# Kernel optimization log

Measured on AMD Instinct MI355X. Metric: run time of the kernel, lower is better.

Reference implementation:

```python
import jax, jax.numpy as jnp
from jax import lax
import numpy as np

SHAPE = (50, 60, 65)   # -> after net: (17, 27, 32), flatten = 14688
NEG = 0.01             # LeakyReLU default slope
B, N = 8, 80000        # batch size, total active voxels


def _lrelu(x):
    return jnp.where(x >= 0, x, NEG * x)


def _sparse_conv(x, w, b, m):
    # Regular (non-submanifold) sparse conv == dense VALID conv on densified
    # input (inactive sites are 0 so they contribute nothing). Output site is
    # active iff any input site in the kernel footprint is active; bias is
    # added only at active output sites.
    k = w.shape[2]
    y = lax.conv_general_dilated(x, w, (1, 1, 1), 'VALID',
                                 dimension_numbers=('NCDHW', 'OIDHW', 'NCDHW'))
    m2 = lax.reduce_window(m, 0.0, lax.max, (1, 1, k, k, k), (1, 1, 1, 1, 1), 'VALID')
    y = jnp.where(m2 > 0, y + b[None, :, None, None, None], 0.0)
    return y, m2


def _sparse_maxpool(x, m, k):
    # spconv SparseMaxPool: max over ACTIVE sites only (inactive excluded, not 0)
    xm = jnp.where(m > 0, x, -jnp.inf)
    p = lax.reduce_window(xm, -jnp.inf, lax.max, (1, 1, k, k, k), (1, 1, 1, 1, 1), 'VALID')
    m2 = lax.reduce_window(m, 0.0, lax.max, (1, 1, k, k, k), (1, 1, 1, 1, 1), 'VALID')
    return jnp.where(m2 > 0, p, 0.0), m2


def setup_inputs() -> dict:
    key = jax.random.key(0)
    ks = jax.random.split(key, 24)
    D, H, W = SHAPE
    features = jax.random.normal(ks[0], (N, 1), dtype=jnp.float32)
    bi = jax.random.randint(ks[1], (N,), 0, B)
    zi = jax.random.randint(ks[2], (N,), 0, D)
    yi = jax.random.randint(ks[3], (N,), 0, H)
    xi = jax.random.randint(ks[4], (N,), 0, W)
    coors = jnp.stack([bi, zi, yi, xi], axis=1).astype(jnp.int32)
    s = 0.05
    p = {}
    p['w1'] = jax.random.normal(ks[5], (32, 1, 4, 4, 4), jnp.float32) * s
    p['b1'] = jax.random.normal(ks[6], (32,), jnp.float32) * s
    p['w2'] = jax.random.normal(ks[7], (32, 32, 4, 4, 4), jnp.float32) * s
    p['b2'] = jax.random.normal(ks[8], (32,), jnp.float32) * s
    p['w3'] = jax.random.normal(ks[9], (32, 32, 4, 4, 4), jnp.float32) * s
    p['b3'] = jax.random.normal(ks[10], (32,), jnp.float32) * s
    p['w4'] = jax.random.normal(ks[11], (32, 32, 4, 4, 4), jnp.float32) * s
    p['b4'] = jax.random.normal(ks[12], (32,), jnp.float32) * s
    p['w5'] = jax.random.normal(ks[13], (32, 32, 4, 4, 4), jnp.float32) * s
    p['b5'] = jax.random.normal(ks[14], (32,), jnp.float32) * s
    p['w6'] = jax.random.normal(ks[15], (32, 32, 4, 4, 4), jnp.float32) * s
    p['b6'] = jax.random.normal(ks[16], (32,), jnp.float32) * s
    p['w7'] = jax.random.normal(ks[17], (1, 32, 4, 4, 4), jnp.float32) * s
    p['b7'] = jax.random.normal(ks[18], (1,), jnp.float32) * s
    p['W8'] = jax.random.normal(ks[19], (14688, 1000), jnp.float32) * 0.01
    p['b8'] = jax.random.normal(ks[20], (1000,), jnp.float32) * s
    p['W9'] = jax.random.normal(ks[21], (1000, 1000), jnp.float32) * 0.03
    p['b9'] = jax.random.normal(ks[22], (1000,), jnp.float32) * s
    p['W10'] = jax.random.normal(ks[23], (1000, 1), jnp.float32) * 0.03
    p['b10'] = jnp.zeros((1,), jnp.float32)
    return dict(features=features, coors=coors, batch_size=B, **p)


def reference(features, coors, batch_size,
              w1, b1, w2, b2, w3, b3, w4, b4, w5, b5, w6, b6, w7, b7,
              W8, b8, W9, b9, W10, b10):
    D, H, W = SHAPE
    bi, zi, yi, xi = coors[:, 0], coors[:, 1], coors[:, 2], coors[:, 3]
    dense = jnp.zeros((batch_size, 1, D, H, W), features.dtype)
    dense = dense.at[bi, 0, zi, yi, xi].set(features[:, 0])
    mask = jnp.zeros((batch_size, 1, D, H, W), features.dtype)
    mask = mask.at[bi, 0, zi, yi, xi].set(1.0)

    x, m = _sparse_conv(dense, w1, b1, mask); x = _lrelu(x)
    x, m = _sparse_conv(x, w2, b2, m);        x = _lrelu(x)
    x, m = _sparse_maxpool(x, m, 5)
    x, m = _sparse_conv(x, w3, b3, m);        x = _lrelu(x)
    x, m = _sparse_conv(x, w4, b4, m);        x = _lrelu(x)
    x, m = _sparse_maxpool(x, m, 5)
    x, m = _sparse_conv(x, w5, b5, m);        x = _lrelu(x)
    x, m = _sparse_conv(x, w6, b6, m);        x = _lrelu(x)
    x, m = _sparse_conv(x, w7, b7, m);        x = _lrelu(x)
    x, m = _sparse_maxpool(x, m, 5)

    # ToDense (inactive sites already 0) + Flatten -> [B, 14688]
    h = x.reshape(x.shape[0], -1)
    h = _lrelu(h @ W8 + b8)
    h = _lrelu(h @ W9 + b9)
    out = _lrelu(h @ W10 + b10)
    return out
```

## Files before the change

### kernel.cpp

```cpp
#include <hip/hip_runtime.h>
#include <cstddef>


#define NEGSLOPE 0.01f
#define NINF (-3.0e38f)

#define TZ 4
#define TY 4
#define TXT 16
#define IZ 7
#define IY 7
#define IX 19
#define NV (IZ*IY*IX)

typedef __attribute__((ext_vector_type(8)))  short  short8;
typedef __attribute__((ext_vector_type(16))) float  floatx16;

__device__ __forceinline__ float lrelu(float v) { return v >= 0.f ? v : NEGSLOPE * v; }

__device__ __forceinline__ unsigned short f2bf(float f) {
  unsigned b = __float_as_uint(f);
  return (unsigned short)((b + 0x7fffu + ((b >> 16) & 1u)) >> 16);
}
__device__ __forceinline__ float bf2f(unsigned short h) {
  return __uint_as_float(((unsigned)h) << 16);
}
__device__ __forceinline__ unsigned splitpair(float a, float b, unsigned& lo) {
  unsigned short ha = f2bf(a), hb = f2bf(b);
  unsigned short la = f2bf(a - bf2f(ha)), lb = f2bf(b - bf2f(hb));
  lo = (unsigned)la | ((unsigned)lb << 16);
  return (unsigned)ha | ((unsigned)hb << 16);
}

__global__ void k_claim(const int* __restrict__ coors, unsigned* __restrict__ claim, int N) {
  int i = blockIdx.x * blockDim.x + threadIdx.x;
  if (i >= N) return;
  int b = coors[4*i], z = coors[4*i+1], y = coors[4*i+2], x = coors[4*i+3];
  int v = ((b*50 + z)*60 + y)*65 + x;
  atomicMax(&claim[v], (unsigned)(i + 1));
}

__global__ void k_scatter(const int* __restrict__ coors, const float* __restrict__ feat,
                          const unsigned* __restrict__ claim,
                          float* __restrict__ x0, float* __restrict__ m0, int N) {
  int i = blockIdx.x * blockDim.x + threadIdx.x;
  if (i >= N) return;
  int b = coors[4*i], z = coors[4*i+1], y = coors[4*i+2], x = coors[4*i+3];
  int v = ((b*50 + z)*60 + y)*65 + x;
  m0[v] = 1.f;
  if (claim[v] == (unsigned)(i + 1)) x0[v] = feat[i];
}

__global__ void k_repack(const float* __restrict__ w, float* __restrict__ wr, int CI, int CO) {
  int i = blockIdx.x * blockDim.x + threadIdx.x;
  int tot = CO * CI * 64;
  if (i >= tot) return;
  int k = i & 63;
  int ci = (i >> 6) % CI;
  int co = i / (64 * CI);
  wr[(k * CI + ci) * CO + co] = w[i];
}

__global__ void k_repack_mfma(const float* __restrict__ w, unsigned short* __restrict__ tbl) {
  int i = blockIdx.x * blockDim.x + threadIdx.x;
  if (i >= 64*4*2*64) return;
  int lane = i & 63; int t = i >> 6;
  int pack = t & 1; t >>= 1;
  int pass = t & 3; int tap = t >> 2;
  int co = lane & 31; int oct = lane >> 5;
#pragma unroll
  for (int j = 0; j < 8; ++j) {
    int k = oct * 8 + j;
    int ci = pass * 8 + (k & 7);
    int part = ((k >> 3) ^ pack) & 1;
    float wv = w[((co * 32 + ci) << 6) + tap];
    unsigned short wh = f2bf(wv);
    unsigned short r = part ? f2bf(wv - bf2f(wh)) : wh;
    tbl[(size_t)i * 8 + j] = r;
  }
}

__global__ void k_dilate(const float* __restrict__ m, float* __restrict__ o,
                         int Zi, int Yi, int Xi, int Zo, int Yo, int Xo, int K, int nI) {
  int gid = blockIdx.x * blockDim.x + threadIdx.x;
  int perOut = Zo * Yo * Xo;
  int tot = nI * perOut;
  if (gid >= tot) return;
  int item = gid / perOut;
  int r = gid - item * perOut;
  int x = r % Xo; int t = r / Xo;
  int y = t % Yo; int z = t / Yo;
  const float* mb = m + (size_t)item * Zi * Yi * Xi;
  float mx = 0.f;
  for (int dz = 0; dz < K; dz++)
    for (int dy = 0; dy < K; dy++) {
      const float* row = mb + (size_t)(((z + dz)*Yi + y + dy)*Xi + x);
      for (int dx = 0; dx < K; dx++) mx = fmaxf(mx, row[dx]);
    }
  o[gid] = mx;
}

__global__ __launch_bounds__(256, 3)
void k_conv32m(const float* __restrict__ in, const unsigned short* __restrict__ tbl,
               const float* __restrict__ bias, const float* __restrict__ mo,
               float* __restrict__ out,
               int Zi, int Yi, int Xi, int Zo, int Yo, int Xo,
               int tilesZ, int tilesY, int tilesX) {
  __shared__ unsigned sU[NV * 12];
  const int perIn = Zi * Yi * Xi;
  const int perOut = Zo * Yo * Xo;
  int bid = blockIdx.x;
  int txi = bid % tilesX; bid /= tilesX;
  int tyi = bid % tilesY; bid /= tilesY;
  int tzi = bid % tilesZ; int item = bid / tilesZ;
  const int z0 = tzi * TZ, y0 = tyi * TY, x0 = txi * TXT;
  const int tid = threadIdx.x;
  const int lane = tid & 63;
  const int col = lane & 31;
  const int oct = lane >> 5;
  const int wv  = tid >> 6;

  int lvBase0, lvBase1;
  {
    int vt0 = (2*wv + 0)*32 + col;
    int vt1 = (2*wv + 1)*32 + col;
    lvBase0 = ((vt0 >> 6)*IY + ((vt0 >> 4) & 3))*IX + (vt0 & 15);
    lvBase1 = ((vt1 >> 6)*IY + ((vt1 >> 4) & 3))*IX + (vt1 & 15);
  }

  floatx16 acc0, acc1;
#pragma unroll
  for (int r = 0; r < 16; ++r) { acc0[r] = 0.f; acc1[r] = 0.f; }

  const float* inb = in + (size_t)item * perIn * 32;
  const char* tb = (const char*)tbl + lane * 16;

#pragma unroll 1
  for (int p = 0; p < 4; ++p) {
    __syncthreads();
    for (int idx = tid; idx < NV; idx += 256) {
      int iz = idx / (IY * IX); int r = idx - iz * (IY * IX);
      int iy = r / IX; int ix = r - iy * IX;
      int gz = z0 + iz, gy = y0 + iy, gx = x0 + ix;
      float4 f0 = make_float4(0.f,0.f,0.f,0.f), f1 = make_float4(0.f,0.f,0.f,0.f);
      if (gz < Zi && gy < Yi && gx < Xi) {
        const float* vp = inb + (size_t)((gz * Yi + gy) * Xi + gx) * 32 + p * 8;
        f0 = *(const float4*)vp;
        f1 = *(const float4*)(vp + 4);
      }
      unsigned l0, l1, l2, l3;
      unsigned h0 = splitpair(f0.x, f0.y, l0);
      unsigned h1 = splitpair(f0.z, f0.w, l1);
      unsigned h2 = splitpair(f1.x, f1.y, l2);
      unsigned h3 = splitpair(f1.z, f1.w, l3);
      uint4 ahv = {h0, h1, h2, h3};
      uint4 alv = {l0, l1, l2, l3};
      ((uint4*)sU)[idx * 3 + 0] = ahv;
      ((uint4*)sU)[idx * 3 + 1] = alv;
    }
    __syncthreads();

    const char* tp = tb + (size_t)p * 2048;
#pragma unroll 2
    for (int tap = 0; tap < 64; ++tap) {
      int kz = tap >> 4, ky = (tap >> 2) & 3, kx = tap & 3;
      int sOff = (kz * IY + ky) * IX + kx;
      short8 b0 = *(const short8*)(tp + (size_t)tap * 8192);
      short8 b1 = *(const short8*)(tp + (size_t)tap * 8192 + 1024);
      short8 a0 = *(const short8*)((const char*)sU + (size_t)(lvBase0 + sOff) * 48 + oct * 16);
      short8 a1 = *(const short8*)((const char*)sU + (size_t)(lvBase1 + sOff) * 48 + oct * 16);
      acc0 = __builtin_amdgcn_mfma_f32_32x32x16_bf16(a0, b0, acc0, 0, 0, 0);
      acc0 = __builtin_amdgcn_mfma_f32_32x32x16_bf16(a0, b1, acc0, 0, 0, 0);
      acc1 = __builtin_amdgcn_mfma_f32_32x32x16_bf16(a1, b0, acc1, 0, 0, 0);
      acc1 = __builtin_amdgcn_mfma_f32_32x32x16_bf16(a1, b1, acc1, 0, 0, 0);
    }
  }

  const float bco = bias[col];
#pragma unroll
  for (int gg = 0; gg < 2; ++gg) {
    int vtb = (2*wv + gg) * 32;
#pragma unroll
    for (int rg = 0; rg < 16; ++rg) {
      int row = (rg & 3) + 8 * (rg >> 2) + 4 * oct;
      int vt = vtb + row;
      int oz = vt >> 6, oy = (vt >> 4) & 3, ox = vt & 15;
      int gz = z0 + oz, gy = y0 + oy, gx = x0 + ox;
      if (gz < Zo && gy < Yo && gx < Xo) {
        int ov = item * perOut + (gz * Yo + gy) * Xo + gx;
        float val = (gg == 0) ? acc0[rg] : acc1[rg];
        bool act = mo[ov] > 0.f;
        out[(size_t)ov * 32 + col] = lrelu(act ? (val + bco) : 0.f);
      }
    }
  }
}

__global__ __launch_bounds__(256, 2)
void k_conv1t(const float* __restrict__ in, const float* __restrict__ wr,
              const float* __restrict__ bias, const float* __restrict__ mo,
              float* __restrict__ out,
              int Zi, int Yi, int Xi, int Zo, int Yo, int Xo,
              int tilesZ, int tilesY, int tilesX) {
  __shared__ float sinf[NV];
  __shared__ float4 wsh[512];
  {
    const float4* wr4 = (const float4*)wr;
    for (int idx = threadIdx.x; idx < 512; idx += 256) wsh[idx] = wr4[idx];
  }
  const int perIn = Zi * Yi * Xi;
  const int perOut = Zo * Yo * Xo;
  int bid = blockIdx.x;
  int txi = bid % tilesX; bid /= tilesX;
  int tyi = bid % tilesY; bid /= tilesY;
  int tzi = bid % tilesZ; int item = bid / tilesZ;
  const int z0 = tzi * TZ, y0 = tyi * TY, x0 = txi * TXT;
  const int tid = threadIdx.x;
  const int ox = tid & 15, oy = (tid >> 4) & 3, oz = tid >> 6;

  const float* inb = in + (size_t)item * perIn;
  for (int idx = tid; idx < NV; idx += 256) {
    int iz = idx / (IY * IX); int r = idx - iz * (IY * IX);
    int iy = r / IX; int ix = r - iy * IX;
    int gz = z0 + iz, gy = y0 + iy, gx = x0 + ix;
    float val = 0.f;
    if (gz < Zi && gy < Yi && gx < Xi)
      val = inb[(size_t)((gz * Yi + gy) * Xi + gx)];
    sinf[idx] = val;
  }
  __syncthreads();

  float4 acc[8];
#pragma unroll
  for (int j = 0; j < 8; ++j) acc[j] = make_float4(0.f, 0.f, 0.f, 0.f);

#pragma unroll 1
  for (int tap = 0; tap < 64; ++tap) {
    int kz = tap >> 4, ky = (tap >> 2) & 3, kx = tap & 3;
    int lv = ((oz + kz) * IY + (oy + ky)) * IX + (ox + kx);
    float av = sinf[lv];
#pragma unroll
    for (int j = 0; j < 8; ++j) {
      float4 wvv = wsh[tap * 8 + j];
      acc[j].x = fmaf(av, wvv.x, acc[j].x);
      acc[j].y = fmaf(av, wvv.y, acc[j].y);
      acc[j].z = fmaf(av, wvv.z, acc[j].z);
      acc[j].w = fmaf(av, wvv.w, acc[j].w);
    }
  }

  int gz = z0 + oz, gy = y0 + oy, gx = x0 + ox;
  if (gz < Zo && gy < Yo && gx < Xo) {
    int ov = item * perOut + (gz * Yo + gy) * Xo + gx;
    bool act = mo[ov] > 0.f;
    const float4* b4 = (const float4*)bias;
    float* op = out + (size_t)ov * 32;
#pragma unroll
    for (int j = 0; j < 8; ++j) {
      float4 r = acc[j]; float4 bj = b4[j];
      r.x = lrelu(act ? (r.x + bj.x) : 0.f);
      r.y = lrelu(act ? (r.y + bj.y) : 0.f);
      r.z = lrelu(act ? (r.z + bj.z) : 0.f);
      r.w = lrelu(act ? (r.w + bj.w) : 0.f);
      *(float4*)(op + j * 4) = r;
    }
  }
}

__global__ __launch_bounds__(256, 2)
void k_conv7t(const float* __restrict__ in, const float* __restrict__ wr,
              const float* __restrict__ bias, const float* __restrict__ mo,
              float* __restrict__ out,
              int Zi, int Yi, int Xi, int Zo, int Yo, int Xo,
              int tilesZ, int tilesY, int tilesX) {
  __shared__ float4 sin4[4][NV];
  __shared__ float4 wsh[512];
  {
    const float4* wr4 = (const float4*)wr;
    for (int idx = threadIdx.x; idx < 512; idx += 256) wsh[idx] = wr4[idx];
  }
  const int perIn = Zi * Yi * Xi;
  const int perOut = Zo * Yo * Xo;
  int bid = blockIdx.x;
  int txi = bid % tilesX; bid /= tilesX;
  int tyi = bid % tilesY; bid /= tilesY;
  int tzi = bid % tilesZ; int item = bid / tilesZ;
  const int z0 = tzi * TZ, y0 = tyi * TY, x0 = txi * TXT;
  const int tid = threadIdx.x;
  const int ox = tid & 15, oy = (tid >> 4) & 3, oz = tid >> 6;

  const float* inb = in + (size_t)item * perIn * 32;
  float acc = 0.f;

#pragma unroll 1
  for (int h = 0; h < 2; ++h) {
    __syncthreads();
    for (int idx = tid; idx < NV * 4; idx += 256) {
      int q = idx / NV; int v = idx - q * NV;
      int iz = v / (IY * IX); int r = v - iz * (IY * IX);
      int iy = r / IX; int ix = r - iy * IX;
      int gz = z0 + iz, gy = y0 + iy, gx = x0 + ix;
      float4 val = make_float4(0.f, 0.f, 0.f, 0.f);
      if (gz < Zi && gy < Yi && gx < Xi)
        val = *(const float4*)(inb + (size_t)((gz * Yi + gy) * Xi + gx) * 32 + h * 16 + q * 4);
      sin4[q][v] = val;
    }
    __syncthreads();
#pragma unroll 1
    for (int tap = 0; tap < 64; ++tap) {
      int kz = tap >> 4, ky = (tap >> 2) & 3, kx = tap & 3;
      int lv = ((oz + kz) * IY + (oy + ky)) * IX + (ox + kx);
      float4 a0 = sin4[0][lv];
      float4 a1 = sin4[1][lv];
      float4 a2 = sin4[2][lv];
      float4 a3 = sin4[3][lv];
      float4 w0 = wsh[tap * 8 + h * 4 + 0];
      float4 w1 = wsh[tap * 8 + h * 4 + 1];
      float4 w2 = wsh[tap * 8 + h * 4 + 2];
      float4 w3 = wsh[tap * 8 + h * 4 + 3];
      acc += a0.x*w0.x + a0.y*w0.y + a0.z*w0.z + a0.w*w0.w
           + a1.x*w1.x + a1.y*w1.y + a1.z*w1.z + a1.w*w1.w
           + a2.x*w2.x + a2.y*w2.y + a2.z*w2.z + a2.w*w2.w
           + a3.x*w3.x + a3.y*w3.y + a3.z*w3.z + a3.w*w3.w;
    }
  }

  int gz = z0 + oz, gy = y0 + oy, gx = x0 + ox;
  if (gz < Zo && gy < Yo && gx < Xo) {
    int ov = item * perOut + (gz * Yo + gy) * Xo + gx;
    bool act = mo[ov] > 0.f;
    out[ov] = lrelu(act ? (acc + bias[0]) : 0.f);
  }
}

__global__ void k_pool_z(const float* __restrict__ in, const float* __restrict__ m,
                         float* __restrict__ out, int Zi, int Yi, int Xi, int Zo, int nI) {
  int gid = blockIdx.x * blockDim.x + threadIdx.x;
  int perOut = Zo * Yi * Xi;
  int tot = nI * perOut * 8;
  if (gid >= tot) return;
  int c4 = gid & 7; int v = gid >> 3;
  int item = v / perOut;
  int r = v - item * perOut;
  int x = r % Xi; int t = r / Xi;
  int y = t % Yi; int z = t / Yi;
  int ib = item * Zi * Yi * Xi;
  float4 acc = {NINF, NINF, NINF, NINF};
  for (int j = 0; j < 5; j++) {
    int vi = ib + ((z + j)*Yi + y)*Xi + x;
    if (m[vi] > 0.f) {
      float4 val = *(const float4*)(in + (size_t)vi*32 + c4*4);
      acc.x = fmaxf(acc.x, val.x); acc.y = fmaxf(acc.y, val.y);
      acc.z = fmaxf(acc.z, val.z); acc.w = fmaxf(acc.w, val.w);
    }
  }
  *(float4*)(out + (size_t)v*32 + c4*4) = acc;
}

__global__ void k_pool_y(const float* __restrict__ in, float* __restrict__ out,
                         int Z, int Yi, int Xi, int Yo, int nI) {
  int gid = blockIdx.x * blockDim.x + threadIdx.x;
  int perOut = Z * Yo * Xi;
  int tot = nI * perOut * 8;
  if (gid >= tot) return;
  int c4 = gid & 7; int v = gid >> 3;
  int item = v / perOut;
  int r = v - item * perOut;
  int x = r % Xi; int t = r / Xi;
  int y = t % Yo; int z = t / Yo;
  int ib = item * Z * Yi * Xi;
  float4 acc = {NINF, NINF, NINF, NINF};
  for (int j = 0; j < 5; j++) {
    int vi = ib + (z*Yi + y + j)*Xi + x;
    float4 val = *(const float4*)(in + (size_t)vi*32 + c4*4);
    acc.x = fmaxf(acc.x, val.x); acc.y = fmaxf(acc.y, val.y);
    acc.z = fmaxf(acc.z, val.z); acc.w = fmaxf(acc.w, val.w);
  }
  *(float4*)(out + (size_t)v*32 + c4*4) = acc;
}

__global__ void k_pool_x(const float* __restrict__ in, const float* __restrict__ mp,
                         float* __restrict__ out, int Z, int Y, int Xi, int Xo, int nI) {
  int gid = blockIdx.x * blockDim.x + threadIdx.x;
  int perOut = Z * Y * Xo;
  int tot = nI * perOut * 8;
  if (gid >= tot) return;
  int c4 = gid & 7; int v = gid >> 3;
  int item = v / perOut;
  int r = v - item * perOut;
  int x = r % Xo; int t = r / Xo;
  int y = t % Y; int z = t / Y;
  int ib = item * Z * Y * Xi;
  float4 acc = {NINF, NINF, NINF, NINF};
  for (int j = 0; j < 5; j++) {
    int vi = ib + (z*Y + y)*Xi + x + j;
    float4 val = *(const float4*)(in + (size_t)vi*32 + c4*4);
    acc.x = fmaxf(acc.x, val.x); acc.y = fmaxf(acc.y, val.y);
    acc.z = fmaxf(acc.z, val.z); acc.w = fmaxf(acc.w, val.w);
  }
  bool act = mp[v] > 0.f;
  float4 rr;
  rr.x = act ? acc.x : 0.f; rr.y = act ? acc.y : 0.f;
  rr.z = act ? acc.z : 0.f; rr.w = act ? acc.w : 0.f;
  *(float4*)(out + (size_t)v*32 + c4*4) = rr;
}

__global__ void k_pool3(const float* __restrict__ xin, const float* __restrict__ m,
                        const float* __restrict__ mp, float* __restrict__ out, int nI) {
  int gid = blockIdx.x * blockDim.x + threadIdx.x;
  int perOut = 17 * 27 * 32;
  int tot = nI * perOut;
  if (gid >= tot) return;
  int item = gid / perOut;
  int r = gid - item * perOut;
  int x = r & 31; int t = r >> 5;
  int y = t % 27; int z = t / 27;
  const float* xb = xin + (size_t)item * 23436;
  const float* mb = m + (size_t)item * 23436;
  float acc = NINF;
  for (int dz = 0; dz < 5; dz++)
    for (int dy = 0; dy < 5; dy++) {
      const float* rowx = xb + (size_t)(((z + dz)*31 + y + dy)*36 + x);
      const float* rowm = mb + (size_t)(((z + dz)*31 + y + dy)*36 + x);
      for (int dx = 0; dx < 5; dx++)
        if (rowm[dx] > 0.f) acc = fmaxf(acc, rowx[dx]);
    }
  out[gid] = (mp[gid] > 0.f) ? acc : 0.f;
}

__global__ __launch_bounds__(256, 4)
void k_fc_part(const float* __restrict__ X, const float* __restrict__ Wm,
               float* __restrict__ part, int K, int Ncol, int Kc) {
  __shared__ float sm[16][16][8];
  int ks = blockIdx.y;
  int k0 = ks * Kc;
  int k1 = k0 + Kc; if (k1 > K) k1 = K;
  int cl = threadIdx.x & 15;
  int kt = threadIdx.x >> 4;
  int col = blockIdx.x * 16 + cl;
  float a0=0.f,a1=0.f,a2=0.f,a3=0.f,a4=0.f,a5=0.f,a6=0.f,a7=0.f;
  if (col < Ncol) {
    for (int k = k0 + kt; k < k1; k += 16) {
      float w = Wm[(size_t)k * Ncol + col];
      a0 += X[0 * K + k] * w; a1 += X[1 * K + k] * w;
      a2 += X[2 * K + k] * w; a3 += X[3 * K + k] * w;
      a4 += X[4 * K + k] * w; a5 += X[5 * K + k] * w;
      a6 += X[6 * K + k] * w; a7 += X[7 * K + k] * w;
    }
  }
  sm[kt][cl][0]=a0; sm[kt][cl][1]=a1; sm[kt][cl][2]=a2; sm[kt][cl][3]=a3;
  sm[kt][cl][4]=a4; sm[kt][cl][5]=a5; sm[kt][cl][6]=a6; sm[kt][cl][7]=a7;
  __syncthreads();
  if (threadIdx.x < 128) {
    int c = threadIdx.x & 15;
    int b = threadIdx.x >> 4;
    float s = 0.f;
#pragma unroll
    for (int k = 0; k < 16; k++) s += sm[k][c][b];
    int cc = blockIdx.x * 16 + c;
    if (cc < Ncol) part[((size_t)ks * 8 + b) * Ncol + cc] = s;
  }
}

__global__ void k_fc_fin(const float* __restrict__ part, int ns,
                         const float* __restrict__ bias, float* __restrict__ out, int Ncol) {
  int i = blockIdx.x * blockDim.x + threadIdx.x;
  if (i >= 8 * Ncol) return;
  int b = i / Ncol;
  int c = i - b * Ncol;
  float s = 0.f;
  for (int ks = 0; ks < ns; ks++) s += part[((size_t)ks * 8 + b) * Ncol + c];
  out[i] = lrelu(s + bias[c]);
}

__global__ __launch_bounds__(256, 4)
void k_fc(const float* __restrict__ X, const float* __restrict__ Wm,
          const float* __restrict__ bias, float* __restrict__ out,
          int K, int Ncol) {
  __shared__ float sm[16][16][8];
  int cl = threadIdx.x & 15;
  int kt = threadIdx.x >> 4;
  int col = blockIdx.x * 16 + cl;
  float a0=0.f,a1=0.f,a2=0.f,a3=0.f,a4=0.f,a5=0.f,a6=0.f,a7=0.f;
  if (col < Ncol) {
    for (int k = kt; k < K; k += 16) {
      float w = Wm[(size_t)k * Ncol + col];
      a0 += X[0 * K + k] * w; a1 += X[1 * K + k] * w;
      a2 += X[2 * K + k] * w; a3 += X[3 * K + k] * w;
      a4 += X[4 * K + k] * w; a5 += X[5 * K + k] * w;
      a6 += X[6 * K + k] * w; a7 += X[7 * K + k] * w;
    }
  }
  sm[kt][cl][0]=a0; sm[kt][cl][1]=a1; sm[kt][cl][2]=a2; sm[kt][cl][3]=a3;
  sm[kt][cl][4]=a4; sm[kt][cl][5]=a5; sm[kt][cl][6]=a6; sm[kt][cl][7]=a7;
  __syncthreads();
  if (threadIdx.x < 128) {
    int c = threadIdx.x & 15;
    int b = threadIdx.x >> 4;
    float s = 0.f;
#pragma unroll
    for (int k = 0; k < 16; k++) s += sm[k][c][b];
    int cc = blockIdx.x * 16 + c;
    if (cc < Ncol) out[b * Ncol + cc] = lrelu(s + bias[cc]);
  }
}

static inline int G256(long long n) { return (int)((n + 255) / 256); }

extern "C" void kernel_launch(void* const* d_in, const int* in_sizes, int n_in,
                              void* d_out, int out_size, void* d_ws, size_t ws_size,
                              hipStream_t stream) {
  const float* feat  = (const float*)d_in[0];
  const int*   coors = (const int*)d_in[1];
  const float* w1 = (const float*)d_in[3];  const float* b1 = (const float*)d_in[4];
  const float* w2 = (const float*)d_in[5];  const float* b2 = (const float*)d_in[6];
  const float* w3 = (const float*)d_in[7];  const float* b3 = (const float*)d_in[8];
  const float* w4 = (const float*)d_in[9];  const float* b4 = (const float*)d_in[10];
  const float* w5 = (const float*)d_in[11]; const float* b5 = (const float*)d_in[12];
  const float* w6 = (const float*)d_in[13]; const float* b6 = (const float*)d_in[14];
  const float* w7 = (const float*)d_in[15]; const float* b7 = (const float*)d_in[16];
  const float* W8 = (const float*)d_in[17]; const float* b8 = (const float*)d_in[18];
  const float* W9 = (const float*)d_in[19]; const float* b9 = (const float*)d_in[20];
  const float* W10= (const float*)d_in[21]; const float* b10= (const float*)d_in[22];
  float* out = (float*)d_out;

  char* ws = (char*)d_ws;
  size_t off = 0;
  auto alloc = [&](size_t nfloats) -> float* {
    float* p = (float*)(ws + off);
    off += ((nfloats * 4 + 1023) / 1024) * 1024;
    return p;
  };

  float* x0  = alloc(1560000);
  float* m0  = alloc(1560000);
  float* m1  = alloc(8 * 166098);
  float* m2  = alloc(8 * 140184);
  float* mp1 = alloc(8 * 110000);
  float* m3  = alloc(8 * 90428);
  float* m4  = alloc(8 * 73304);
  float* mp2 = alloc(8 * 54000);
  float* m5  = alloc(8 * 41958);
  float* m6  = alloc(8 * 31824);
  float* m7  = alloc(8 * 23436);
  float* mp3 = alloc(8 * 14688);
  float* p3  = alloc(8 * 14688);
  float* wr1 = alloc(2048);
  float* wr7 = alloc(2048);
  unsigned short* tb2 = (unsigned short*)alloc(131072);
  unsigned short* tb3 = (unsigned short*)alloc(131072);
  unsigned short* tb4 = (unsigned short*)alloc(131072);
  unsigned short* tb5 = (unsigned short*)alloc(131072);
  unsigned short* tb6 = (unsigned short*)alloc(131072);
  float* part= alloc(64000);
  float* h8  = alloc(8000);
  float* h9  = alloc(8000);
  size_t fixedOff = off;

  const size_t perItemAB = ((size_t)5315136*4 + 1023)/1024*1024
                         + ((size_t)4485888*4 + 1023)/1024*1024
                         + ((size_t)23436*4 + 1023)/1024*1024;
  int G = 0;
  for (int g : {8, 4, 2, 1})
    if (fixedOff + (size_t)g * perItemAB <= ws_size) { G = g; break; }
  if (G == 0) return;

  float* A  = alloc((size_t)G * 5315136);
  float* Bb = alloc((size_t)G * 4485888);
  float* x7 = alloc((size_t)G * 23436);
  unsigned* claim = (unsigned*)A;

  hipMemsetAsync(claim, 0, 1560000 * 4, stream);
  hipMemsetAsync(x0,    0, 1560000 * 4, stream);
  hipMemsetAsync(m0,    0, 1560000 * 4, stream);

  k_repack<<<G256(32*1*64),  256, 0, stream>>>(w1, wr1, 1, 32);
  k_repack<<<G256(1*32*64),  256, 0, stream>>>(w7, wr7, 32, 1);
  k_repack_mfma<<<128, 256, 0, stream>>>(w2, tb2);
  k_repack_mfma<<<128, 256, 0, stream>>>(w3, tb3);
  k_repack_mfma<<<128, 256, 0, stream>>>(w4, tb4);
  k_repack_mfma<<<128, 256, 0, stream>>>(w5, tb5);
  k_repack_mfma<<<128, 256, 0, stream>>>(w6, tb6);

  const int N = 80000;
  k_claim  <<<G256(N), 256, 0, stream>>>(coors, claim, N);
  k_scatter<<<G256(N), 256, 0, stream>>>(coors, feat, claim, x0, m0, N);

  k_dilate<<<G256(8*166098), 256, 0, stream>>>(m0,  m1,  50,60,65, 47,57,62, 4, 8);
  k_dilate<<<G256(8*140184), 256, 0, stream>>>(m1,  m2,  47,57,62, 44,54,59, 4, 8);
  k_dilate<<<G256(8*110000), 256, 0, stream>>>(m2,  mp1, 44,54,59, 40,50,55, 5, 8);
  k_dilate<<<G256(8*90428),  256, 0, stream>>>(mp1, m3,  40,50,55, 37,47,52, 4, 8);
  k_dilate<<<G256(8*73304),  256, 0, stream>>>(m3,  m4,  37,47,52, 34,44,49, 4, 8);
  k_dilate<<<G256(8*54000),  256, 0, stream>>>(m4,  mp2, 34,44,49, 30,40,45, 5, 8);
  k_dilate<<<G256(8*41958),  256, 0, stream>>>(mp2, m5,  30,40,45, 27,37,42, 4, 8);
  k_dilate<<<G256(8*31824),  256, 0, stream>>>(m5,  m6,  27,37,42, 24,34,39, 4, 8);
  k_dilate<<<G256(8*23436),  256, 0, stream>>>(m6,  m7,  24,34,39, 21,31,36, 4, 8);
  k_dilate<<<G256(8*14688),  256, 0, stream>>>(m7,  mp3, 21,31,36, 17,27,32, 5, 8);

  auto conv32 = [&](const float* in, const unsigned short* tbl, const float* bias,
                    const float* mo, float* o,
                    int Zi, int Yi, int Xi, int Zo, int Yo, int Xo, int nI) {
    int tz = (Zo + TZ - 1) / TZ, ty = (Yo + TY - 1) / TY, tx = (Xo + TXT - 1) / TXT;
    k_conv32m<<<nI * tz * ty * tx, 256, 0, stream>>>(
        in, tbl, bias, mo, o, Zi, Yi, Xi, Zo, Yo, Xo, tz, ty, tx);
  };

  for (int g0 = 0; g0 < 8; g0 += G) {
    const float* x0g  = x0  + (size_t)g0 * 195000;
    const float* m1g  = m1  + (size_t)g0 * 166098;
    const float* m2g  = m2  + (size_t)g0 * 140184;
    const float* mp1g = mp1 + (size_t)g0 * 110000;
    const float* m3g  = m3  + (size_t)g0 * 90428;
    const float* m4g  = m4  + (size_t)g0 * 73304;
    const float* mp2g = mp2 + (size_t)g0 * 54000;
    const float* m5g  = m5  + (size_t)g0 * 41958;
    const float* m6g  = m6  + (size_t)g0 * 31824;
    const float* m7g  = m7  + (size_t)g0 * 23436;
    const float* mp3g = mp3 + (size_t)g0 * 14688;

    {
      int tz = (47 + TZ - 1) / TZ, ty = (57 + TY - 1) / TY, tx = (62 + TXT - 1) / TXT;
      k_conv1t<<<G * tz * ty * tx, 256, 0, stream>>>(
          x0g, wr1, b1, m1g, A, 50,60,65, 47,57,62, tz, ty, tx);
    }
    conv32(A, tb2, b2, m2g, Bb, 47,57,62, 44,54,59, G);
    k_pool_z<<<G256((long long)G*127440*8), 256, 0, stream>>>(Bb, m2g,  A,  44,54,59, 40, G);
    k_pool_y<<<G256((long long)G*118000*8), 256, 0, stream>>>(A,  Bb, 40,54,59, 50, G);
    k_pool_x<<<G256((long long)G*110000*8), 256, 0, stream>>>(Bb, mp1g, A,  40,50,59, 55, G);
    conv32(A, tb3, b3, m3g, Bb, 40,50,55, 37,47,52, G);
    conv32(Bb, tb4, b4, m4g, A, 37,47,52, 34,44,49, G);
    k_pool_z<<<G256((long long)G*64680*8), 256, 0, stream>>>(A,  m4g,  Bb, 34,44,49, 30, G);
    k_pool_y<<<G256((long long)G*58800*8), 256, 0, stream>>>(Bb, A,  30,44,49, 40, G);
    k_pool_x<<<G256((long long)G*54000*8), 256, 0, stream>>>(A,  mp2g, Bb, 30,40,49, 45, G);
    conv32(Bb, tb5, b5, m5g, A, 30,40,45, 27,37,42, G);
    conv32(A, tb6, b6, m6g, Bb, 27,37,42, 24,34,39, G);
    {
      int tz = (21 + TZ - 1) / TZ, ty = (31 + TY - 1) / TY, tx = (36 + TXT - 1) / TXT;
      k_conv7t<<<G * tz * ty * tx, 256, 0, stream>>>(
          Bb, wr7, b7, m7g, x7, 24,34,39, 21,31,36, tz, ty, tx);
    }
    k_pool3<<<G256((long long)G*14688), 256, 0, stream>>>(
        x7, m7g, mp3g, p3 + (size_t)g0 * 14688, G);
  }

  k_fc_part<<<dim3(63, 8), 256, 0, stream>>>(p3, W8, part, 14688, 1000, 1836);
  k_fc_fin <<<G256(8000), 256, 0, stream>>>(part, 8, b8, h8, 1000);
  k_fc_part<<<dim3(63, 4), 256, 0, stream>>>(h8, W9, part, 1000, 1000, 250);
  k_fc_fin <<<G256(8000), 256, 0, stream>>>(part, 4, b9, h9, 1000);
  k_fc<<<1, 256, 0, stream>>>(h9, W10, b10, out, 1000, 1);
}
```

Before: 3.700 ms.

## Shrink conv32 tile to 4x4x8 per block and separate mask dilation

The MFMA conv kernel now computes a 4x4x8 output tile per block, one 32-voxel MFMA tile per wave instead of two, with a smaller shared-memory halo (7x7x11). Occupancy is raised to 6 blocks per CU. The intent is more parallelism and lower LDS and register pressure, at the cost of more halo re-loading and bf16 splitting per output. Separately, the K^3 mask dilation is split into three 1-D max passes (z, y, x) through temporary buffers, cutting reads per output from K^3 to 3K at the cost of two extra launches per dilation.

```diff
diff --git a/kernel.cpp b/kernel.cpp
--- a/kernel.cpp
+++ b/kernel.cpp
@@ -12,6 +12,13 @@
 #define IY 7
 #define IX 19
 #define NV (IZ*IY*IX)
+
+#define CZ 4
+#define CY 4
+#define CX 8
+#define HIY 7
+#define HIX 11
+#define HNV (7*HIY*HIX)
 
 typedef __attribute__((ext_vector_type(8)))  short  short8;
 typedef __attribute__((ext_vector_type(16))) float  floatx16;
@@ -80,57 +87,76 @@
   }
 }
 
-__global__ void k_dilate(const float* __restrict__ m, float* __restrict__ o,
-                         int Zi, int Yi, int Xi, int Zo, int Yo, int Xo, int K, int nI) {
+__global__ void kd_z(const float* __restrict__ in, float* __restrict__ o,
+                     int Zi, int Yi, int Xi, int Zo, int K, int nI) {
+  int gid = blockIdx.x * blockDim.x + threadIdx.x;
+  int perOut = Zo * Yi * Xi;
+  if (gid >= nI * perOut) return;
+  int item = gid / perOut;
+  int r = gid - item * perOut;
+  int x = r % Xi; int t = r / Xi;
+  int y = t % Yi; int z = t / Yi;
+  const float* ib = in + (size_t)item * Zi * Yi * Xi;
+  float mx = 0.f;
+  for (int d = 0; d < K; d++) mx = fmaxf(mx, ib[((z + d) * Yi + y) * Xi + x]);
+  o[gid] = mx;
+}
+
+__global__ void kd_y(const float* __restrict__ in, float* __restrict__ o,
+                     int Zo, int Yi, int Xi, int Yo, int K, int nI) {
+  int gid = blockIdx.x * blockDim.x + threadIdx.x;
+  int perOut = Zo * Yo * Xi;
+  if (gid >= nI * perOut) return;
+  int item = gid / perOut;
+  int r = gid - item * perOut;
+  int x = r % Xi; int t = r / Xi;
+  int y = t % Yo; int z = t / Yo;
+  const float* ib = in + (size_t)item * Zo * Yi * Xi;
+  float mx = 0.f;
+  for (int d = 0; d < K; d++) mx = fmaxf(mx, ib[(z * Yi + y + d) * Xi + x]);
+  o[gid] = mx;
+}
+
+__global__ void kd_x(const float* __restrict__ in, float* __restrict__ o,
+                     int Zo, int Yo, int Xi, int Xo, int K, int nI) {
   int gid = blockIdx.x * blockDim.x + threadIdx.x;
   int perOut = Zo * Yo * Xo;
-  int tot = nI * perOut;
-  if (gid >= tot) return;
+  if (gid >= nI * perOut) return;
   int item = gid / perOut;
   int r = gid - item * perOut;
   int x = r % Xo; int t = r / Xo;
   int y = t % Yo; int z = t / Yo;
-  const float* mb = m + (size_t)item * Zi * Yi * Xi;
+  const float* ib = in + (size_t)item * Zo * Yo * Xi;
   float mx = 0.f;
-  for (int dz = 0; dz < K; dz++)
-    for (int dy = 0; dy < K; dy++) {
-      const float* row = mb + (size_t)(((z + dz)*Yi + y + dy)*Xi + x);
-      for (int dx = 0; dx < K; dx++) mx = fmaxf(mx, row[dx]);
-    }
+  for (int d = 0; d < K; d++) mx = fmaxf(mx, ib[(z * Yo + y) * Xi + x + d]);
   o[gid] = mx;
 }
 
-__global__ __launch_bounds__(256, 3)
+__global__ __launch_bounds__(256, 6)
 void k_conv32m(const float* __restrict__ in, const unsigned short* __restrict__ tbl,
                const float* __restrict__ bias, const float* __restrict__ mo,
                float* __restrict__ out,
                int Zi, int Yi, int Xi, int Zo, int Yo, int Xo,
                int tilesZ, int tilesY, int tilesX) {
-  __shared__ unsigned sU[NV * 12];
+  __shared__ unsigned sU[HNV * 12];
   const int perIn = Zi * Yi * Xi;
   const int perOut = Zo * Yo * Xo;
   int bid = blockIdx.x;
   int txi = bid % tilesX; bid /= tilesX;
   int tyi = bid % tilesY; bid /= tilesY;
   int tzi = bid % tilesZ; int item = bid / tilesZ;
-  const int z0 = tzi * TZ, y0 = tyi * TY, x0 = txi * TXT;
+  const int z0 = tzi * CZ, y0 = tyi * CY, x0 = txi * CX;
   const int tid = threadIdx.x;
   const int lane = tid & 63;
   const int col = lane & 31;
   const int oct = lane >> 5;
   const int wv  = tid >> 6;
 
-  int lvBase0, lvBase1;
-  {
-    int vt0 = (2*wv + 0)*32 + col;
-    int vt1 = (2*wv + 1)*32 + col;
-    lvBase0 = ((vt0 >> 6)*IY + ((vt0 >> 4) & 3))*IX + (vt0 & 15);
-    lvBase1 = ((vt1 >> 6)*IY + ((vt1 >> 4) & 3))*IX + (vt1 & 15);
-  }
-
-  floatx16 acc0, acc1;
-#pragma unroll
-  for (int r = 0; r < 16; ++r) { acc0[r] = 0.f; acc1[r] = 0.f; }
+  const int lvBase = ((wv) * HIY + ((col >> 3) & 3)) * HIX + (col & 7);
+
+  floatx16 acc;
+#pragma unroll
+  for (int r = 0; r < 16; ++r) acc[r] = 0.f;
 
   const float* inb = in + (size_t)item * perIn * 32;
   const char* tb = (const char*)tbl + lane * 16;
@@ -138,9 +164,9 @@
 #pragma unroll 1
   for (int p = 0; p < 4; ++p) {
     __syncthreads();
-    for (int idx = tid; idx < NV; idx += 256) {
-      int iz = idx / (IY * IX); int r = idx - iz * (IY * IX);
-      int iy = r / IX; int ix = r - iy * IX;
+    for (int idx = tid; idx < HNV; idx += 256) {
+      int iz = idx / (HIY * HIX); int r = idx - iz * (HIY * HIX);
+      int iy = r / HIX; int ix = r - iy * HIX;
       int gz = z0 + iz, gy = y0 + iy, gx = x0 + ix;
       float4 f0 = make_float4(0.f,0.f,0.f,0.f), f1 = make_float4(0.f,0.f,0.f,0.f);
       if (gz < Zi && gy < Yi && gx < Xi) {
@@ -164,34 +190,25 @@
 #pragma unroll 2
     for (int tap = 0; tap < 64; ++tap) {
       int kz = tap >> 4, ky = (tap >> 2) & 3, kx = tap & 3;
-      int sOff = (kz * IY + ky) * IX + kx;
+      int sOff = (kz * HIY + ky) * HIX + kx;
       short8 b0 = *(const short8*)(tp + (size_t)tap * 8192);
       short8 b1 = *(const short8*)(tp + (size_t)tap * 8192 + 1024);
-      short8 a0 = *(const short8*)((const char*)sU + (size_t)(lvBase0 + sOff) * 48 + oct * 16);
-      short8 a1 = *(const short8*)((const char*)sU + (size_t)(lvBase1 + sOff) * 48 + oct * 16);
-      acc0 = __builtin_amdgcn_mfma_f32_32x32x16_bf16(a0, b0, acc0, 0, 0, 0);
-      acc0 = __builtin_amdgcn_mfma_f32_32x32x16_bf16(a0, b1, acc0, 0, 0, 0);
-      acc1 = __builtin_amdgcn_mfma_f32_32x32x16_bf16(a1, b0, acc1, 0, 0, 0);
-      acc1 = __builtin_amdgcn_mfma_f32_32x32x16_bf16(a1, b1, acc1, 0, 0, 0);
+      short8 a0 = *(const short8*)((const char*)sU + (size_t)(lvBase + sOff) * 48 + oct * 16);
+      acc = __builtin_amdgcn_mfma_f32_32x32x16_bf16(a0, b0, acc, 0, 0, 0);
+      acc = __builtin_amdgcn_mfma_f32_32x32x16_bf16(a0, b1, acc, 0, 0, 0);
     }
   }
 
   const float bco = bias[col];
 #pragma unroll
-  for (int gg = 0; gg < 2; ++gg) {
-    int vtb = (2*wv + gg) * 32;
-#pragma unroll
-    for (int rg = 0; rg < 16; ++rg) {
-      int row = (rg & 3) + 8 * (rg >> 2) + 4 * oct;
-      int vt = vtb + row;
-      int oz = vt >> 6, oy = (vt >> 4) & 3, ox = vt & 15;
-      int gz = z0 + oz, gy = y0 + oy, gx = x0 + ox;
-      if (gz < Zo && gy < Yo && gx < Xo) {
-        int ov = item * perOut + (gz * Yo + gy) * Xo + gx;
-        float val = (gg == 0) ? acc0[rg] : acc1[rg];
-        bool act = mo[ov] > 0.f;
-        out[(size_t)ov * 32 + col] = lrelu(act ? (val + bco) : 0.f);
-      }
+  for (int rg = 0; rg < 16; ++rg) {
+    int row = (rg & 3) + 8 * (rg >> 2) + 4 * oct;
+    int oz = wv, oy = (row >> 3) & 3, ox = row & 7;
+    int gz = z0 + oz, gy = y0 + oy, gx = x0 + ox;
+    if (gz < Zo && gy < Yo && gx < Xo) {
+      int ov = item * perOut + (gz * Yo + gy) * Xo + gx;
+      bool act = mo[ov] > 0.f;
+      out[(size_t)ov * 32 + col] = lrelu(act ? (acc[rg] + bco) : 0.f);
     }
   }
 }
@@ -545,6 +562,8 @@
   float* m7  = alloc(8 * 23436);
   float* mp3 = alloc(8 * 14688);
   float* p3  = alloc(8 * 14688);
+  float* dt1 = alloc(8 * 183300);
+  float* dt2 = alloc(8 * 174135);
   float* wr1 = alloc(2048);
   float* wr7 = alloc(2048);
   unsigned short* tb2 = (unsigned short*)alloc(131072);
@@ -586,21 +605,27 @@
   k_claim  <<<G256(N), 256, 0, stream>>>(coors, claim, N);
   k_scatter<<<G256(N), 256, 0, stream>>>(coors, feat, claim, x0, m0, N);
 
-  k_dilate<<<G256(8*166098), 256, 0, stream>>>(m0,  m1,  50,60,65, 47,57,62, 4, 8);
-  k_dilate<<<G256(8*140184), 256, 0, stream>>>(m1,  m2,  47,57,62, 44,54,59, 4, 8);
-  k_dilate<<<G256(8*110000), 256, 0, stream>>>(m2,  mp1, 44,54,59, 40,50,55, 5, 8);
-  k_dilate<<<G256(8*90428),  256, 0, stream>>>(mp1, m3,  40,50,55, 37,47,52, 4, 8);
-  k_dilate<<<G256(8*73304),  256, 0, stream>>>(m3,  m4,  37,47,52, 34,44,49, 4, 8);
-  k_dilate<<<G256(8*54000),  256, 0, stream>>>(m4,  mp2, 34,44,49, 30,40,45, 5, 8);
-  k_dilate<<<G256(8*41958),  256, 0, stream>>>(mp2, m5,  30,40,45, 27,37,42, 4, 8);
-  k_dilate<<<G256(8*31824),  256, 0, stream>>>(m5,  m6,  27,37,42, 24,34,39, 4, 8);
-  k_dilate<<<G256(8*23436),  256, 0, stream>>>(m6,  m7,  24,34,39, 21,31,36, 4, 8);
-  k_dilate<<<G256(8*14688),  256, 0, stream>>>(m7,  mp3, 21,31,36, 17,27,32, 5, 8);
+  auto dil3 = [&](const float* src, float* dst,
+                  int Zi, int Yi, int Xi, int Zo, int Yo, int Xo, int K) {
+    kd_z<<<G256((long long)8*Zo*Yi*Xi), 256, 0, stream>>>(src, dt1, Zi,Yi,Xi, Zo, K, 8);
+    kd_y<<<G256((long long)8*Zo*Yo*Xi), 256, 0, stream>>>(dt1, dt2, Zo,Yi,Xi, Yo, K, 8);
+    kd_x<<<G256((long long)8*Zo*Yo*Xo), 256, 0, stream>>>(dt2, dst, Zo,Yo,Xi, Xo, K, 8);
+  };
+  dil3(m0,  m1,  50,60,65, 47,57,62, 4);
+  dil3(m1,  m2,  47,57,62, 44,54,59, 4);
+  dil3(m2,  mp1, 44,54,59, 40,50,55, 5);
+  dil3(mp1, m3,  40,50,55, 37,47,52, 4);
+  dil3(m3,  m4,  37,47,52, 34,44,49, 4);
+  dil3(m4,  mp2, 34,44,49, 30,40,45, 5);
+  dil3(mp2, m5,  30,40,45, 27,37,42, 4);
+  dil3(m5,  m6,  27,37,42, 24,34,39, 4);
+  dil3(m6,  m7,  24,34,39, 21,31,36, 4);
+  dil3(m7,  mp3, 21,31,36, 17,27,32, 5);
 
   auto conv32 = [&](const float* in, const unsigned short* tbl, const float* bias,
                     const float* mo, float* o,
                     int Zi, int Yi, int Xi, int Zo, int Yo, int Xo, int nI) {
-    int tz = (Zo + TZ - 1) / TZ, ty = (Yo + TY - 1) / TY, tx = (Xo + TXT - 1) / TXT;
+    int tz = (Zo + CZ - 1) / CZ, ty = (Yo + CY - 1) / CY, tx = (Xo + CX - 1) / CX;
     k_conv32m<<<nI * tz * ty * tx, 256, 0, stream>>>(
         in, tbl, bias, mo, o, Zi, Yi, Xi, Zo, Yo, Xo, tz, ty, tx);
   };
```

After: 3.574 ms. -3.4%, faster.
